# Performance work log

Hardware: AMD Instinct MI355X
Metric: run time of the kernel (lower is better)

Reference implementation:

```python
import jax, jax.numpy as jnp
import numpy as np

NUM_LAYERS = 9
HIDDEN = 3


def _param_indices(hidden, num_layers):
    # Mirrors DistributionFreeModel.calculate_parameter_indices
    offset = 3 + (num_layers - 2) * (hidden + 2)
    idx = [((0 * hidden, 1 * hidden), (1 * hidden, 2 * hidden), (2 * hidden, 3 * hidden))]
    for o in range(3, offset, hidden + 2):
        idx.append((
            (o * hidden, (o + hidden) * hidden),
            ((o + hidden) * hidden, (o + hidden + 1) * hidden),
            ((o + hidden + 1) * hidden, (o + hidden + 2) * hidden),
        ))
    idx.append(((offset * hidden, (offset + 1) * hidden),
                ((offset + 1) * hidden, (offset + 1) * hidden + 1),
                None))
    return idx


def _cdf(inputs, parameters, hidden=HIDDEN, num_layers=NUM_LAYERS):
    # inputs: [B, F]; parameters: [F, P]
    out = inputs[..., None]  # [B, F, 1]
    for li, (wi, bi, si) in enumerate(_param_indices(hidden, num_layers)):
        w = parameters[..., wi[0]:wi[1]]
        b = parameters[..., bi[0]:bi[1]]
        if li == 0:
            w = w.reshape(w.shape[:-1] + (hidden, 1))
        elif li == num_layers - 1:
            w = w.reshape(w.shape[:-1] + (1, hidden))
        else:
            w = w.reshape(w.shape[:-1] + (hidden, hidden))
        w = jax.nn.softplus(w)
        # per-feature tiny matmul, broadcast over batch: [B,F,f] x [F,d,f] -> [B,F,d]
        out = jnp.einsum('...f,...df->...d', out, w) + b
        if si is not None:
            s = jnp.tanh(parameters[..., si[0]:si[1]])
            out = out + s * jnp.tanh(out)
    return jax.nn.sigmoid(out)[..., 0]  # squeeze last dim -> [B, F]


def setup_inputs() -> dict:
    key = jax.random.key(0)
    k1, k2 = jax.random.split(key)
    B, F = 32768, 512
    P = (NUM_LAYERS - 2) * HIDDEN ** 2 + 2 * NUM_LAYERS * HIDDEN + 1  # 118
    inputs = jax.random.normal(k1, (B, F), dtype=jnp.float32)
    parameters = jax.random.normal(k2, (F, P), dtype=jnp.float32)
    return {"inputs": inputs, "parameters": parameters}


def reference(inputs, parameters):
    return _cdf(inputs, parameters)
```

## Files before the change

### kernel.cpp

```cpp
#include <hip/hip_runtime.h>
#include <math.h>

#define NF 512
#define NP 118
#define NPPAD 126
#define FT 32
#define BLOCK_ROWS 64
#define TBL_N 2048
#define WS_NEED ((size_t)(NPPAD * NF + 2 * TBL_N) * sizeof(float))

typedef float v2f __attribute__((ext_vector_type(2)));

__device__ __forceinline__ v2f pk_fma(v2f a, v2f b, v2f c) {
    return __builtin_elementwise_fma(a, b, c);
}
__device__ __forceinline__ v2f splat2(float v) { v2f r; r.x = v; r.y = v; return r; }

__device__ __forceinline__ float fast_rcp(float x) { return __builtin_amdgcn_rcpf(x); }

__device__ __forceinline__ v2f tanh_lut2(v2f x, const v2f* __restrict__ tbl) {
    v2f xi = pk_fma(x, splat2(128.0f), splat2(1024.0f));
    float q0 = __builtin_amdgcn_fmed3f(xi.x, 0.0f, 2047.0f);
    float q1 = __builtin_amdgcn_fmed3f(xi.y, 0.0f, 2047.0f);
    v2f sc0 = tbl[(int)q0];
    v2f sc1 = tbl[(int)q1];
    v2f r;
    r.x = fmaf(x.x, sc0.x, sc0.y);
    r.y = fmaf(x.y, sc1.x, sc1.y);
    return r;
}

__device__ __forceinline__ float transform_one(float v, int j) {
    int cls;
    if (j < 3) cls = 0;
    else if (j < 6) cls = 1;
    else if (j < 9) cls = 2;
    else if (j < 114) { int k = (j - 9) % 15; cls = (k < 9) ? 0 : ((k < 12) ? 1 : 2); }
    else if (j < 117) cls = 0;
    else cls = 1;
    if (cls == 0) return fmaxf(v, 0.0f) + log1pf(expf(-fabsf(v)));
    if (cls == 2) return tanhf(v);
    return v;
}

__device__ __forceinline__ bool map_padded(int jp, int* j) {
    if (jp < 9) { *j = jp; return true; }
    if (jp == 9) return false;
    if (jp < 122) {
        int k = (jp - 10) & 15, li = (jp - 10) >> 4;
        if (k == 15) return false;
        *j = 9 + 15 * li + k;
        return true;
    }
    *j = 114 + (jp - 122);
    return true;
}

__device__ __forceinline__ void tbl_entry(int bin, float* s, float* c) {
    if (bin == 0)              { *s = 0.0f; *c = -1.0f; }
    else if (bin == TBL_N - 1) { *s = 0.0f; *c =  1.0f; }
    else {
        float xl = (float)(bin - 1024) * (1.0f / 128.0f);
        float t0 = tanhf(xl), t1 = tanhf(xl + 1.0f / 128.0f);
        float sl = (t1 - t0) * 128.0f;
        *s = sl; *c = fmaf(-sl, xl, t0);
    }
}

__global__ void xform_kernel(const float* __restrict__ p, float* __restrict__ t) {
    int idx = blockIdx.x * 256 + threadIdx.x;
    if (idx < NPPAD * NF) {
        int jp = idx / NF, f = idx - jp * NF;
        int j; float v = 0.0f;
        if (map_padded(jp, &j)) v = transform_one(p[f * NP + j], j);
        t[idx] = v;
    } else if (idx < NPPAD * NF + TBL_N) {
        int bin = idx - NPPAD * NF;
        float s, c;
        tbl_entry(bin, &s, &c);
        t[NPPAD * NF + 2 * bin]     = s;
        t[NPPAD * NF + 2 * bin + 1] = c;
    }
}

template <bool FUSE_XFORM>
__global__ __launch_bounds__(256)
void cdf_kernel(const float* __restrict__ x, const float* __restrict__ prm,
                float* __restrict__ out) {
    __shared__ float ldsp[NPPAD * FT];
    __shared__ v2f   tblv[TBL_N];
    const int tid = threadIdx.x;
    const int fi  = tid & (FT - 1);
    const int rg  = tid >> 5;
    const int f0  = blockIdx.x * FT;
    const int b0  = blockIdx.y * BLOCK_ROWS + rg * 8;
    const int f   = f0 + fi;

    if constexpr (FUSE_XFORM) {
        for (int idx = tid; idx < NPPAD * FT; idx += 256) {
            int jp = idx >> 5, fl = idx & (FT - 1);
            int j; float v = 0.0f;
            if (map_padded(jp, &j)) v = transform_one(prm[(f0 + fl) * NP + j], j);
            ldsp[(jp >> 1) * (2 * FT) + fl * 2 + (jp & 1)] = v;
        }
        float* tf = (float*)tblv;
        for (int bin = tid; bin < TBL_N; bin += 256) {
            float s, c; tbl_entry(bin, &s, &c);
            tf[2 * bin] = s; tf[2 * bin + 1] = c;
        }
    } else {
        for (int idx = tid; idx < NPPAD * FT; idx += 256) {
            int jp = idx >> 5, fl = idx & (FT - 1);
            ldsp[(jp >> 1) * (2 * FT) + fl * 2 + (jp & 1)] = prm[jp * NF + f0 + fl];
        }
        float* tf = (float*)tblv;
        const float* tw = prm + NPPAD * NF;
        for (int idx = tid; idx < 2 * TBL_N; idx += 256)
            tf[idx] = tw[idx];
    }

    v2f xin[4];
#pragma unroll
    for (int r = 0; r < 4; ++r) {
        xin[r].x = x[(b0 + 2 * r)     * NF + f];
        xin[r].y = x[(b0 + 2 * r + 1) * NF + f];
    }

    __syncthreads();

    const float* Pp = ldsp + fi * 2;
#define PRMV(JP) (*reinterpret_cast<const v2f*>(Pp + (JP) * FT))

    v2f h0[4], h1[4], h2[4];
    {
        v2f p01 = PRMV(0), p23 = PRMV(2), p45 = PRMV(4), p67 = PRMV(6), p8p = PRMV(8);
        const float w0 = p01.x, w1 = p01.y, w2 = p23.x;
        const float c0 = p23.y, c1 = p45.x, c2 = p45.y;
        const float s0 = p67.x, s1 = p67.y, s2 = p8p.x;
#pragma unroll
        for (int r = 0; r < 4; ++r) {
            v2f a0 = pk_fma(xin[r], splat2(w0), splat2(c0));
            v2f a1 = pk_fma(xin[r], splat2(w1), splat2(c1));
            v2f a2 = pk_fma(xin[r], splat2(w2), splat2(c2));
            h0[r] = pk_fma(splat2(s0), tanh_lut2(a0, tblv), a0);
            h1[r] = pk_fma(splat2(s1), tanh_lut2(a1, tblv), a1);
            h2[r] = pk_fma(splat2(s2), tanh_lut2(a2, tblv), a2);
        }
    }
#pragma unroll
    for (int li = 1; li < 8; ++li) {
        const int bp = 10 + 16 * (li - 1);
        v2f q0 = PRMV(bp + 0), q1 = PRMV(bp + 2), q2 = PRMV(bp + 4), q3 = PRMV(bp + 6);
        v2f q4 = PRMV(bp + 8), q5 = PRMV(bp + 10), q6 = PRMV(bp + 12), q7 = PRMV(bp + 14);
        const float w00 = q0.x, w01 = q0.y, w02 = q1.x;
        const float w10 = q1.y, w11 = q2.x, w12 = q2.y;
        const float w20 = q3.x, w21 = q3.y, w22 = q4.x;
        const float c0  = q4.y, c1  = q5.x, c2  = q5.y;
        const float s0  = q6.x, s1  = q6.y, s2  = q7.x;
#pragma unroll
        for (int r = 0; r < 4; ++r) {
            v2f a0 = pk_fma(h0[r], splat2(w00), pk_fma(h1[r], splat2(w01), pk_fma(h2[r], splat2(w02), splat2(c0))));
            v2f a1 = pk_fma(h0[r], splat2(w10), pk_fma(h1[r], splat2(w11), pk_fma(h2[r], splat2(w12), splat2(c1))));
            v2f a2 = pk_fma(h0[r], splat2(w20), pk_fma(h1[r], splat2(w21), pk_fma(h2[r], splat2(w22), splat2(c2))));
            h0[r] = pk_fma(splat2(s0), tanh_lut2(a0, tblv), a0);
            h1[r] = pk_fma(splat2(s1), tanh_lut2(a1, tblv), a1);
            h2[r] = pk_fma(splat2(s2), tanh_lut2(a2, tblv), a2);
        }
    }
    {
        v2f q0 = PRMV(122), q1 = PRMV(124);
        const float w0 = q0.x, w1 = q0.y, w2 = q1.x, cb = q1.y;
#pragma unroll
        for (int r = 0; r < 4; ++r) {
            v2f a = pk_fma(h0[r], splat2(w0),
                    pk_fma(h1[r], splat2(w1),
                    pk_fma(h2[r], splat2(w2), splat2(cb))));
            out[(b0 + 2 * r)     * NF + f] = fast_rcp(1.0f + __expf(-a.x));
            out[(b0 + 2 * r + 1) * NF + f] = fast_rcp(1.0f + __expf(-a.y));
        }
    }
#undef PRMV
}

extern "C" void kernel_launch(void* const* d_in, const int* in_sizes, int n_in,
                              void* d_out, int out_size, void* d_ws, size_t ws_size,
                              hipStream_t stream) {
    const float* x = (const float*)d_in[0];
    const float* p = (const float*)d_in[1];
    float* out = (float*)d_out;

    const int B = in_sizes[0] / NF;
    dim3 grid(NF / FT, B / BLOCK_ROWS);
    dim3 block(256);

    if (ws_size >= WS_NEED) {
        float* t = (float*)d_ws;
        int total = NPPAD * NF + TBL_N;
        xform_kernel<<<(total + 255) / 256, 256, 0, stream>>>(p, t);
        cdf_kernel<false><<<grid, block, 0, stream>>>(x, t, out);
    } else {
        cdf_kernel<true><<<grid, block, 0, stream>>>(x, p, out);
    }
}
```

Measured before the change: 111.4 us.

## Use op_sel packed FMAs, tanh-based sigmoid, and narrower feature tiles

Replaces the compiler-generated splat+packed FMA sequences with inline-asm v_pk_fma_f32 using op_sel to broadcast a scalar parameter straight from a packed register pair, which avoids the extra moves. The final sigmoid is now computed as 0.5*tanh(x/2)+0.5 through the existing LUT, with the final weights pre-halved, instead of exp plus reciprocal. The tile shape changes to 16 features by 128 rows, launch bounds ask for 6 waves per SIMD, and the table bins are shifted by half a bin. The risks are lower LUT accuracy in the output sigmoid and fragile inline asm that the compiler cannot schedule around.

```diff
diff --git a/kernel.cpp b/kernel.cpp
--- a/kernel.cpp
+++ b/kernel.cpp
@@ -4,22 +4,33 @@
 #define NF 512
 #define NP 118
 #define NPPAD 126
-#define FT 32
-#define BLOCK_ROWS 64
+#define FT 16
+#define ROWS 8
+#define BLOCK_ROWS 128
 #define TBL_N 2048
 #define WS_NEED ((size_t)(NPPAD * NF + 2 * TBL_N) * sizeof(float))
 
 typedef float v2f __attribute__((ext_vector_type(2)));
 
-__device__ __forceinline__ v2f pk_fma(v2f a, v2f b, v2f c) {
-    return __builtin_elementwise_fma(a, b, c);
-}
-__device__ __forceinline__ v2f splat2(float v) { v2f r; r.x = v; r.y = v; return r; }
-
-__device__ __forceinline__ float fast_rcp(float x) { return __builtin_amdgcn_rcpf(x); }
-
-__device__ __forceinline__ v2f tanh_lut2(v2f x, const v2f* __restrict__ tbl) {
-    v2f xi = pk_fma(x, splat2(128.0f), splat2(1024.0f));
+__device__ __forceinline__ v2f f_PP(v2f a, v2f b, v2f c) {
+    v2f d; asm("v_pk_fma_f32 %0, %1, %2, %3" : "=v"(d) : "v"(a), "v"(b), "v"(c)); return d;
+}
+__device__ __forceinline__ v2f f_LP(v2f a, v2f b, v2f c) {
+    v2f d; asm("v_pk_fma_f32 %0, %1, %2, %3 op_sel_hi:[1,0,1]" : "=v"(d) : "v"(a), "v"(b), "v"(c)); return d;
+}
+__device__ __forceinline__ v2f f_HP(v2f a, v2f b, v2f c) {
+    v2f d; asm("v_pk_fma_f32 %0, %1, %2, %3 op_sel:[0,1,0] op_sel_hi:[1,1,1]" : "=v"(d) : "v"(a), "v"(b), "v"(c)); return d;
+}
+__device__ __forceinline__ v2f f_LH(v2f a, v2f b, v2f c) {
+    v2f d; asm("v_pk_fma_f32 %0, %1, %2, %3 op_sel:[0,0,1] op_sel_hi:[1,0,1]" : "=v"(d) : "v"(a), "v"(b), "v"(c)); return d;
+}
+__device__ __forceinline__ v2f f_HL(v2f a, v2f b, v2f c) {
+    v2f d; asm("v_pk_fma_f32 %0, %1, %2, %3 op_sel:[0,1,0] op_sel_hi:[1,1,0]" : "=v"(d) : "v"(a), "v"(b), "v"(c)); return d;
+}
+
+__device__ __forceinline__ v2f tanh_pair(v2f x, const v2f* __restrict__ tbl,
+                                         v2f K128, v2f K1024) {
+    v2f xi = f_PP(x, K128, K1024);
     float q0 = __builtin_amdgcn_fmed3f(xi.x, 0.0f, 2047.0f);
     float q1 = __builtin_amdgcn_fmed3f(xi.y, 0.0f, 2047.0f);
     v2f sc0 = tbl[(int)q0];
@@ -56,24 +67,28 @@
     return true;
 }
 
-__device__ __forceinline__ void tbl_entry(int bin, float* s, float* c) {
-    if (bin == 0)              { *s = 0.0f; *c = -1.0f; }
-    else if (bin == TBL_N - 1) { *s = 0.0f; *c =  1.0f; }
-    else {
-        float xl = (float)(bin - 1024) * (1.0f / 128.0f);
-        float t0 = tanhf(xl), t1 = tanhf(xl + 1.0f / 128.0f);
-        float sl = (t1 - t0) * 128.0f;
-        *s = sl; *c = fmaf(-sl, xl, t0);
-    }
+__device__ __forceinline__ float transform_padded(const float* __restrict__ prow, int jp) {
+    int j;
+    if (!map_padded(jp, &j)) return 0.0f;
+    float v = transform_one(prow[j], j);
+    if (jp >= 122) v *= 0.5f;
+    return v;
+}
+
+__device__ __forceinline__ void tbl_entry(int b, float* s, float* c) {
+    float xl = (float)b * (1.0f / 128.0f) - (1024.5f / 128.0f);
+    float xr = xl + (1.0f / 128.0f);
+    float t0 = tanhf(xl), t1 = tanhf(xr);
+    float sl = (t1 - t0) * 128.0f;
+    *s = sl;
+    *c = fmaf(-sl, xl, t0);
 }
 
 __global__ void xform_kernel(const float* __restrict__ p, float* __restrict__ t) {
     int idx = blockIdx.x * 256 + threadIdx.x;
     if (idx < NPPAD * NF) {
         int jp = idx / NF, f = idx - jp * NF;
-        int j; float v = 0.0f;
-        if (map_padded(jp, &j)) v = transform_one(p[f * NP + j], j);
-        t[idx] = v;
+        t[idx] = transform_padded(p + f * NP, jp);
     } else if (idx < NPPAD * NF + TBL_N) {
         int bin = idx - NPPAD * NF;
         float s, c;
@@ -84,24 +99,23 @@
 }
 
 template <bool FUSE_XFORM>
-__global__ __launch_bounds__(256)
+__global__ __launch_bounds__(256, 6)
 void cdf_kernel(const float* __restrict__ x, const float* __restrict__ prm,
                 float* __restrict__ out) {
     __shared__ float ldsp[NPPAD * FT];
     __shared__ v2f   tblv[TBL_N];
     const int tid = threadIdx.x;
     const int fi  = tid & (FT - 1);
-    const int rg  = tid >> 5;
+    const int rg  = tid >> 4;
     const int f0  = blockIdx.x * FT;
-    const int b0  = blockIdx.y * BLOCK_ROWS + rg * 8;
+    const int b0  = blockIdx.y * BLOCK_ROWS + rg * ROWS;
     const int f   = f0 + fi;
 
     if constexpr (FUSE_XFORM) {
         for (int idx = tid; idx < NPPAD * FT; idx += 256) {
-            int jp = idx >> 5, fl = idx & (FT - 1);
-            int j; float v = 0.0f;
-            if (map_padded(jp, &j)) v = transform_one(prm[(f0 + fl) * NP + j], j);
-            ldsp[(jp >> 1) * (2 * FT) + fl * 2 + (jp & 1)] = v;
+            int jp = idx >> 4, fl = idx & (FT - 1);
+            ldsp[(jp >> 1) * (2 * FT) + fl * 2 + (jp & 1)] =
+                transform_padded(prm + (f0 + fl) * NP, jp);
         }
         float* tf = (float*)tblv;
         for (int bin = tid; bin < TBL_N; bin += 256) {
@@ -110,7 +124,7 @@
         }
     } else {
         for (int idx = tid; idx < NPPAD * FT; idx += 256) {
-            int jp = idx >> 5, fl = idx & (FT - 1);
+            int jp = idx >> 4, fl = idx & (FT - 1);
             ldsp[(jp >> 1) * (2 * FT) + fl * 2 + (jp & 1)] = prm[jp * NF + f0 + fl];
         }
         float* tf = (float*)tblv;
@@ -128,23 +142,27 @@
 
     __syncthreads();
 
+    const v2f K128  = {128.0f, 128.0f};
+    const v2f K1024 = {1024.5f, 1024.5f};
+    const v2f Khalf = {0.5f, 0.5f};
+
     const float* Pp = ldsp + fi * 2;
 #define PRMV(JP) (*reinterpret_cast<const v2f*>(Pp + (JP) * FT))
 
     v2f h0[4], h1[4], h2[4];
     {
-        v2f p01 = PRMV(0), p23 = PRMV(2), p45 = PRMV(4), p67 = PRMV(6), p8p = PRMV(8);
-        const float w0 = p01.x, w1 = p01.y, w2 = p23.x;
-        const float c0 = p23.y, c1 = p45.x, c2 = p45.y;
-        const float s0 = p67.x, s1 = p67.y, s2 = p8p.x;
+        v2f q0 = PRMV(0), q1 = PRMV(2), q2 = PRMV(4), q3 = PRMV(6), q4 = PRMV(8);
 #pragma unroll
         for (int r = 0; r < 4; ++r) {
-            v2f a0 = pk_fma(xin[r], splat2(w0), splat2(c0));
-            v2f a1 = pk_fma(xin[r], splat2(w1), splat2(c1));
-            v2f a2 = pk_fma(xin[r], splat2(w2), splat2(c2));
-            h0[r] = pk_fma(splat2(s0), tanh_lut2(a0, tblv), a0);
-            h1[r] = pk_fma(splat2(s1), tanh_lut2(a1, tblv), a1);
-            h2[r] = pk_fma(splat2(s2), tanh_lut2(a2, tblv), a2);
+            v2f a0 = f_LH(xin[r], q0, q1);
+            v2f a1 = f_HL(xin[r], q0, q2);
+            v2f a2 = f_LH(xin[r], q1, q2);
+            v2f T0 = tanh_pair(a0, tblv, K128, K1024);
+            v2f T1 = tanh_pair(a1, tblv, K128, K1024);
+            v2f T2 = tanh_pair(a2, tblv, K128, K1024);
+            h0[r] = f_LP(T0, q3, a0);
+            h1[r] = f_HP(T1, q3, a1);
+            h2[r] = f_LP(T2, q4, a2);
         }
     }
 #pragma unroll
@@ -152,31 +170,36 @@
         const int bp = 10 + 16 * (li - 1);
         v2f q0 = PRMV(bp + 0), q1 = PRMV(bp + 2), q2 = PRMV(bp + 4), q3 = PRMV(bp + 6);
         v2f q4 = PRMV(bp + 8), q5 = PRMV(bp + 10), q6 = PRMV(bp + 12), q7 = PRMV(bp + 14);
-        const float w00 = q0.x, w01 = q0.y, w02 = q1.x;
-        const float w10 = q1.y, w11 = q2.x, w12 = q2.y;
-        const float w20 = q3.x, w21 = q3.y, w22 = q4.x;
-        const float c0  = q4.y, c1  = q5.x, c2  = q5.y;
-        const float s0  = q6.x, s1  = q6.y, s2  = q7.x;
 #pragma unroll
         for (int r = 0; r < 4; ++r) {
-            v2f a0 = pk_fma(h0[r], splat2(w00), pk_fma(h1[r], splat2(w01), pk_fma(h2[r], splat2(w02), splat2(c0))));
-            v2f a1 = pk_fma(h0[r], splat2(w10), pk_fma(h1[r], splat2(w11), pk_fma(h2[r], splat2(w12), splat2(c1))));
-            v2f a2 = pk_fma(h0[r], splat2(w20), pk_fma(h1[r], splat2(w21), pk_fma(h2[r], splat2(w22), splat2(c2))));
-            h0[r] = pk_fma(splat2(s0), tanh_lut2(a0, tblv), a0);
-            h1[r] = pk_fma(splat2(s1), tanh_lut2(a1, tblv), a1);
-            h2[r] = pk_fma(splat2(s2), tanh_lut2(a2, tblv), a2);
+            v2f t0 = f_LH(h0[r], q0, q4);
+            t0     = f_HP(h1[r], q0, t0);
+            v2f a0 = f_LP(h2[r], q1, t0);
+            v2f t1 = f_HL(h0[r], q1, q5);
+            t1     = f_LP(h1[r], q2, t1);
+            v2f a1 = f_HP(h2[r], q2, t1);
+            v2f t2 = f_LH(h0[r], q3, q5);
+            t2     = f_HP(h1[r], q3, t2);
+            v2f a2 = f_LP(h2[r], q4, t2);
+            v2f T0 = tanh_pair(a0, tblv, K128, K1024);
+            v2f T1 = tanh_pair(a1, tblv, K128, K1024);
+            v2f T2 = tanh_pair(a2, tblv, K128, K1024);
+            h0[r] = f_LP(T0, q6, a0);
+            h1[r] = f_HP(T1, q6, a1);
+            h2[r] = f_LP(T2, q7, a2);
         }
     }
     {
-        v2f q0 = PRMV(122), q1 = PRMV(124);
-        const float w0 = q0.x, w1 = q0.y, w2 = q1.x, cb = q1.y;
+        v2f q8 = PRMV(122), q9 = PRMV(124);
 #pragma unroll
         for (int r = 0; r < 4; ++r) {
-            v2f a = pk_fma(h0[r], splat2(w0),
-                    pk_fma(h1[r], splat2(w1),
-                    pk_fma(h2[r], splat2(w2), splat2(cb))));
-            out[(b0 + 2 * r)     * NF + f] = fast_rcp(1.0f + __expf(-a.x));
-            out[(b0 + 2 * r + 1) * NF + f] = fast_rcp(1.0f + __expf(-a.y));
+            v2f a = f_LH(h0[r], q8, q9);
+            a     = f_HP(h1[r], q8, a);
+            a     = f_LP(h2[r], q9, a);
+            v2f T = tanh_pair(a, tblv, K128, K1024);
+            v2f o = f_PP(T, Khalf, Khalf);
+            out[(b0 + 2 * r)     * NF + f] = o.x;
+            out[(b0 + 2 * r + 1) * NF + f] = o.y;
         }
     }
 #undef PRMV
```

Result: faster. 104.9 us (-5.8%).
